# Kernel optimization log

Hardware: AMD Instinct MI355X
Metric: run time of the kernel (lower is better)

Reference implementation:

```python
import jax, jax.numpy as jnp
import numpy as np

B, N, CIN, CV, D, H, HD, W, SHIFT = 1024, 192, 63, 27, 256, 8, 32, 8, 4
DEPTH, MLP = 2, 256  # mlp_dim = int(embed_dim * mlp_ratio) = 256


def setup_inputs() -> dict:
    key = jax.random.key(0)
    ks = iter(jax.random.split(key, 64))
    def w(*shape):
        return jax.random.normal(next(ks), shape, jnp.float32) * 0.02
    z = lambda *s: jnp.zeros(s, jnp.float32)
    o = lambda *s: jnp.ones(s, jnp.float32)
    return {
        'input_pts': jax.random.normal(next(ks), (B, N, CIN), jnp.float32),
        'input_views': jax.random.normal(next(ks), (B, CV), jnp.float32),
        'w_in': w(CIN, D), 'b_in': z(D),
        'ln_in_s': o(D), 'ln_in_b': z(D),
        'ln1_s': o(DEPTH, D), 'ln1_b': z(DEPTH, D),
        'wq': w(DEPTH, D, H, HD), 'bq': z(DEPTH, H, HD),
        'wk': w(DEPTH, D, H, HD), 'bk': z(DEPTH, H, HD),
        'wv': w(DEPTH, D, H, HD), 'bv': z(DEPTH, H, HD),
        'wo': w(DEPTH, H, HD, D), 'bo': z(DEPTH, D),
        'ln2_s': o(DEPTH, D), 'ln2_b': z(DEPTH, D),
        'w_mlp1': w(DEPTH, D, MLP), 'b_mlp1': z(DEPTH, MLP),
        'w_mlp2': w(DEPTH, MLP, D), 'b_mlp2': z(DEPTH, D),
        'w_skip': w(DEPTH, CIN + D, D), 'b_skip': z(DEPTH, D),
        'ln_f_s': o(D), 'ln_f_b': z(D),
        'w_alpha': w(D, 1), 'b_alpha': z(1),
        'w_feat': w(D, D), 'b_feat': z(D),
        'w_rgb1': w(D + CV, D // 2), 'b_rgb1': z(D // 2),
        'w_rgb2': w(D // 2, 3), 'b_rgb2': z(3),
    }


def _ln(x, s, b, eps=1e-6):
    m = jnp.mean(x, -1, keepdims=True)
    v = jnp.mean(jnp.square(x - m), -1, keepdims=True)
    return (x - m) * jax.lax.rsqrt(v + eps) * s + b


def _pos_embed(n, d):
    pos = jnp.arange(n, dtype=jnp.float32)[:, None]
    i = jnp.arange(d)
    ang = pos / jnp.power(10000.0, (2 * (i // 2)).astype(jnp.float32) / d)
    return jnp.where(i % 2 == 0, jnp.sin(ang), jnp.cos(ang))[None]  # [1, n, d]


def _block(x, shifted, ln1_s, ln1_b, wq, bq, wk, bk, wv, bv, wo, bo,
           ln2_s, ln2_b, w1, b1, w2, b2):
    b, n, c = x.shape
    y = _ln(x, ln1_s, ln1_b)
    if shifted:
        y = jnp.roll(y, -SHIFT, axis=1)
    yw = y.reshape(b * (n // W), W, c)  # window partition
    q = jnp.einsum('bnc,chd->bnhd', yw, wq) + bq
    k = jnp.einsum('bnc,chd->bnhd', yw, wk) + bk
    v = jnp.einsum('bnc,chd->bnhd', yw, wv) + bv
    scale = np.float32(1.0 / np.sqrt(HD))
    a = jax.nn.softmax(jnp.einsum('bqhd,bkhd->bhqk', q * scale, k), axis=-1)
    o = jnp.einsum('bhqk,bkhd->bqhd', a, v)
    o = jnp.einsum('bqhd,hdc->bqc', o, wo) + bo
    o = o.reshape(b, n, c)  # window reverse
    if shifted:
        o = jnp.roll(o, SHIFT, axis=1)
    x = x + o
    y = _ln(x, ln2_s, ln2_b)
    y = jax.nn.gelu(jnp.einsum('bnc,cm->bnm', y, w1) + b1)
    y = jnp.einsum('bnm,mc->bnc', y, w2) + b2
    return x + y


def reference(input_pts, input_views, w_in, b_in, ln_in_s, ln_in_b,
              ln1_s, ln1_b, wq, bq, wk, bk, wv, bv, wo, bo, ln2_s, ln2_b,
              w_mlp1, b_mlp1, w_mlp2, b_mlp2, w_skip, b_skip,
              ln_f_s, ln_f_b, w_alpha, b_alpha, w_feat, b_feat,
              w_rgb1, b_rgb1, w_rgb2, b_rgb2):
    x = input_pts @ w_in + b_in
    x = _ln(x, ln_in_s, ln_in_b)
    x = x + _pos_embed(x.shape[1], x.shape[2])
    for i in range(DEPTH):  # shift on odd layers; skips = [0, 1]
        x = _block(x, i % 2 == 1, ln1_s[i], ln1_b[i], wq[i], bq[i], wk[i], bk[i],
                   wv[i], bv[i], wo[i], bo[i], ln2_s[i], ln2_b[i],
                   w_mlp1[i], b_mlp1[i], w_mlp2[i], b_mlp2[i])
        x = jax.nn.gelu(jnp.concatenate([input_pts, x], -1) @ w_skip[i] + b_skip[i])
    h = _ln(x, ln_f_s, ln_f_b)
    alpha = h @ w_alpha + b_alpha
    feature = h @ w_feat + b_feat
    views = jnp.repeat(input_views[:, None, :], h.shape[1], axis=1)
    hr = jnp.concatenate([feature, views], -1)
    rgb = jax.nn.gelu(hr @ w_rgb1 + b_rgb1) @ w_rgb2 + b_rgb2
    return rgb, alpha
```

## Files before the change

kernel.cpp:

```cpp
#include <hip/hip_runtime.h>
#include <hip/hip_bf16.h>
#include <math.h>

typedef __hip_bfloat16 bf16;
typedef __attribute__((ext_vector_type(8))) short short8;
typedef __attribute__((ext_vector_type(4))) float f32x4;

#define T_TOK 196608
#define NSEQ  192
#define DMODEL 256
#define CHUNKS 4
#define CHUNKM (T_TOK/CHUNKS)

__device__ __forceinline__ float cvt(float v){ return v; }
__device__ __forceinline__ float cvt(bf16 v){ return __bfloat162float(v); }
__device__ __forceinline__ short bfbits(float f){
  bf16 h = __float2bfloat16(f); return *reinterpret_cast<short*>(&h);
}
__device__ __forceinline__ float bfu(unsigned short v){ return __uint_as_float(((unsigned)v) << 16); }

__device__ __forceinline__ float gelu_f(float x){
  const float k0 = 0.7978845608028654f;
  float u = k0*(x + 0.044715f*x*x*x);
  return x / (1.f + __expf(-2.f*u));
}

__device__ __forceinline__ void barrier_lgkm(){
  asm volatile("s_waitcnt lgkmcnt(0)" ::: "memory");
  __builtin_amdgcn_s_barrier();
  asm volatile("" ::: "memory");
}

__global__ __launch_bounds__(256) void pe_kernel(float* __restrict__ PE){
  int n = blockIdx.x, d = threadIdx.x;
  float e = (float)(2*(d>>1)) / 256.f;
  float ang = (float)n * powf(10000.f, -e);
  PE[n*DMODEL + d] = (d & 1) ? cosf(ang) : sinf(ang);
}

__global__ __launch_bounds__(256) void w2b_kernel(
    const float* __restrict__ src, bf16* __restrict__ dst,
    int K, int N, int KL, int dstStride, int kOff, const float* __restrict__ scale)
{
  int idx = blockIdx.x*256 + threadIdx.x;
  if (idx >= N*KL) return;
  int n = idx / KL, k = idx - n*KL;
  float v = 0.f;
  if (k < K){
    v = src[(size_t)k*N + n];
    if (scale) v *= scale[k];
  }
  dst[(size_t)n*dstStride + kOff + k] = __float2bfloat16(v);
}

__global__ __launch_bounds__(256) void ucalc_kernel(
    const float* __restrict__ W, const float* __restrict__ lnS,
    const float* __restrict__ lnB, const float* __restrict__ bias,
    float* __restrict__ u, float* __restrict__ wB, int K, int N)
{
  __shared__ float pu[4], pb[4];
  const int n = blockIdx.x;
  const int k = threadIdx.x;
  float su = 0.f, sb = 0.f;
  if (k < K){
    float w = W[(size_t)k*N + n];
    su = cvt(__float2bfloat16(lnS[k]*w));
    sb = lnB[k]*w;
  }
  #pragma unroll
  for (int off = 32; off; off >>= 1){
    su += __shfl_xor(su, off, 64);
    sb += __shfl_xor(sb, off, 64);
  }
  int lane = k & 63, wv = k >> 6;
  if (lane == 0){ pu[wv] = su; pb[wv] = sb; }
  __syncthreads();
  if (k == 0){
    u[n]  = pu[0]+pu[1]+pu[2]+pu[3];
    wB[n] = pb[0]+pb[1]+pb[2]+pb[3] + bias[n];
  }
}

__global__ __launch_bounds__(256) void pts2b_kernel(
    const float* __restrict__ src, bf16* __restrict__ dst)
{
  int idx = blockIdx.x*256 + threadIdx.x;
  int t = idx >> 6, k = idx & 63;
  dst[idx] = __float2bfloat16(k < 63 ? src[(size_t)t*63 + k] : 0.f);
}

__global__ __launch_bounds__(256) void views2b_kernel(
    const float* __restrict__ src, bf16* __restrict__ dst)
{
  int idx = blockIdx.x*256 + threadIdx.x;
  int t = idx >> 5, k = idx & 31;
  dst[idx] = __float2bfloat16(k < 27 ? src[(size_t)t*27 + k] : 0.f);
}

__global__ __launch_bounds__(256) void ln_pe_kernel(
    bf16* __restrict__ X, const float* __restrict__ s, const float* __restrict__ b,
    const float* __restrict__ PE, float* __restrict__ s1o, float* __restrict__ s2o)
{
  const int lane = threadIdx.x & 63, w = threadIdx.x >> 6;
  const size_t t = (size_t)blockIdx.x * 4 + w;
  const int n = (int)(t % NSEQ);
  const int c = lane * 4;

  ushort4 u = *reinterpret_cast<const ushort4*>(X + t*DMODEL + c);
  float x0 = bfu(u.x), x1 = bfu(u.y), x2 = bfu(u.z), x3 = bfu(u.w);

  float sx = x0 + x1 + x2 + x3;
  float sq = x0*x0 + x1*x1 + x2*x2 + x3*x3;
  #pragma unroll
  for (int off = 32; off; off >>= 1){
    sx += __shfl_xor(sx, off, 64);
    sq += __shfl_xor(sq, off, 64);
  }
  float mean = sx * (1.f/256.f);
  float var  = sq * (1.f/256.f) - mean*mean;
  float rstd = rsqrtf(var + 1e-6f);

  float4 sv = *reinterpret_cast<const float4*>(s + c);
  float4 bv = *reinterpret_cast<const float4*>(b + c);
  float4 pv = *reinterpret_cast<const float4*>(PE + n*DMODEL + c);

  float y0 = (x0 - mean)*rstd*sv.x + bv.x + pv.x;
  float y1 = (x1 - mean)*rstd*sv.y + bv.y + pv.y;
  float y2 = (x2 - mean)*rstd*sv.z + bv.z + pv.z;
  float y3 = (x3 - mean)*rstd*sv.w + bv.w + pv.w;

  ushort4 o;
  o.x = (unsigned short)bfbits(y0);
  o.y = (unsigned short)bfbits(y1);
  o.z = (unsigned short)bfbits(y2);
  o.w = (unsigned short)bfbits(y3);
  *reinterpret_cast<ushort4*>(X + t*DMODEL + c) = o;

  float sy  = y0 + y1 + y2 + y3;
  float syq = y0*y0 + y1*y1 + y2*y2 + y3*y3;
  #pragma unroll
  for (int off = 32; off; off >>= 1){
    sy  += __shfl_xor(sy,  off, 64);
    syq += __shfl_xor(syq, off, 64);
  }
  if (lane == 0){ s1o[t] = sy; s2o[t] = syq; }
}

template<int MODE, bool LNF, bool ADD, bool GELU, bool STATS>
__global__ __launch_bounds__(256) void gemm_mfma(
    const bf16* __restrict__ A1, int lda1,
    const bf16* __restrict__ A2, int lda2, int SB, int aOff,
    const float* __restrict__ s1i, const float* __restrict__ s2i,
    const float* __restrict__ uvec,
    const bf16* __restrict__ WT, int Kpad, const float* __restrict__ bias,
    bf16* __restrict__ C, int ldc, size_t segStride, int cOff, int rollShift,
    float* __restrict__ s1o, float* __restrict__ s2o)
{
  __shared__ short buf[17408];
  short* As0 = buf;
  short* As1 = buf + 5120;
  short* Cs  = buf;
  __shared__ float sScale[128], sAlpha[128];

  const int tid = threadIdx.x;
  const int lane = tid & 63, wid = tid >> 6;
  const int wm = wid >> 1, wn = wid & 1;
  const int col16 = lane & 15, quad = lane >> 4;
  const int sm = tid >> 1, half = tid & 1;
  const int m0 = blockIdx.y * 128, n0 = blockIdx.x * 128;

  f32x4 acc[4][4];
  #pragma unroll
  for (int i = 0; i < 4; i++)
    #pragma unroll
    for (int j = 0; j < 4; j++) acc[i][j] = (f32x4){0.f,0.f,0.f,0.f};

  int row = m0 + sm;
  if (MODE == 0 && rollShift){
    int bb = row / NSEQ;
    int n  = row - bb*NSEQ;
    n += rollShift; if (n >= NSEQ) n -= NSEQ;
    row = bb*NSEQ + n;
  }
  const size_t arow = (size_t)aOff + row;
  const size_t arow2 = (MODE == 3) ? (arow / NSEQ) : arow;

  if (LNF && tid < 128){
    int r2 = m0 + tid;
    if (rollShift){
      int bb = r2 / NSEQ, n = r2 - bb*NSEQ;
      n += rollShift; if (n >= NSEQ) n -= NSEQ;
      r2 = bb*NSEQ + n;
    }
    size_t r = (size_t)aOff + r2;
    float m1 = s1i[r] * (1.f/256.f);
    float m2 = s2i[r] * (1.f/256.f);
    float rs = rsqrtf(m2 - m1*m1 + 1e-6f);
    sScale[tid] = rs;
    sAlpha[tid] = -m1*rs;
  }

  auto loadA = [&](int k0, uint4& u0, uint4& u1){
    const int gk = k0 + half*16;
    const bf16* src;
    if (MODE == 0) src = A1 + arow*(size_t)lda1 + gk;
    else src = (gk < SB) ? (A1 + arow*(size_t)lda1 + gk)
                         : (A2 + arow2*(size_t)lda2 + (gk - SB));
    u0 = *(const uint4*)(src);
    u1 = *(const uint4*)(src + 8);
  };
  auto writeA = [&](short* dst, const uint4& u0, const uint4& u1){
    *(uint4*)&dst[sm*40 + half*16]     = u0;
    *(uint4*)&dst[sm*40 + half*16 + 8] = u1;
  };

  uint4 p0, p1;
  loadA(0, p0, p1);
  writeA(As0, p0, p1);
  if (Kpad > 32) loadA(32, p0, p1);
  barrier_lgkm();

  int cur = 0;
  for (int k0 = 0; k0 < Kpad; k0 += 32){
    const short* Asc = cur ? As1 : As0;
    short8 afr[4];
    #pragma unroll
    for (int mi = 0; mi < 4; mi++)
      afr[mi] = *(const short8*)&Asc[(wm*64 + mi*16 + col16)*40 + quad*8];
    short8 bfr[4];
    #pragma unroll
    for (int ni = 0; ni < 4; ni++)
      bfr[ni] = *(const short8*)((const short*)WT
                 + (size_t)(n0 + wn*64 + ni*16 + col16)*Kpad + k0 + quad*8);
    #pragma unroll
    for (int mi = 0; mi < 4; mi++)
      #pragma unroll
      for (int ni = 0; ni < 4; ni++)
        acc[mi][ni] = __builtin_amdgcn_mfma_f32_16x16x32_bf16(
            afr[mi], bfr[ni], acc[mi][ni], 0, 0, 0);
    if (k0 + 32 < Kpad){
      short* Asn = cur ? As0 : As1;
      writeA(Asn, p0, p1);
      if (k0 + 64 < Kpad) loadA(k0+64, p0, p1);
    }
    barrier_lgkm();
    cur ^= 1;
  }

  #pragma unroll
  for (int ni = 0; ni < 4; ni++){
    int ncol = wn*64 + ni*16 + col16;
    float bv = bias[n0 + ncol];
    float uv = LNF ? uvec[n0 + ncol] : 0.f;
    #pragma unroll
    for (int mi = 0; mi < 4; mi++){
      f32x4 a = acc[mi][ni];
      #pragma unroll
      for (int r = 0; r < 4; r++){
        int lrow = wm*64 + mi*16 + quad*4 + r;
        float val;
        if (LNF) val = sScale[lrow]*a[r] + sAlpha[lrow]*uv + bv;
        else     val = a[r] + bv;
        if (GELU) val = gelu_f(val);
        Cs[lrow*136 + ncol] = bfbits(val);
      }
    }
  }
  __syncthreads();

  const int seg = n0 >> 8;
  const int nb  = n0 & 255;
  const int orow = tid >> 4;
  const int ocol = (tid & 15) * 8;
  #pragma unroll
  for (int p = 0; p < 8; p++){
    int lrow = p*16 + orow;
    size_t mrow = (size_t)cOff + m0 + lrow;
    short8 v = *(const short8*)&Cs[lrow*136 + ocol];
    bf16* dst = C + (size_t)seg*segStride + mrow*ldc + nb + ocol;
    float rowSum = 0.f, rowSq = 0.f;
    if (ADD){
      short8 c = *(const short8*)dst;
      short8 o;
      #pragma unroll
      for (int e = 0; e < 8; e++){
        bf16 va, ca;
        *reinterpret_cast<short*>(&va) = v[e];
        *reinterpret_cast<short*>(&ca) = c[e];
        float f = cvt(va) + cvt(ca);
        o[e] = bfbits(f);
        if (STATS){ rowSum += f; rowSq += f*f; }
      }
      *(short8*)dst = o;
    } else {
      if (STATS){
        #pragma unroll
        for (int e = 0; e < 8; e++){
          bf16 va; *reinterpret_cast<short*>(&va) = v[e];
          float f = cvt(va);
          rowSum += f; rowSq += f*f;
        }
      }
      *(short8*)dst = v;
    }
    if (STATS){
      #pragma unroll
      for (int mk = 1; mk <= 8; mk <<= 1){
        rowSum += __shfl_xor(rowSum, mk, 64);
        rowSq  += __shfl_xor(rowSq,  mk, 64);
      }
      if ((tid & 15) == 0){
        atomicAdd(&s1o[mrow], rowSum);
        atomicAdd(&s2o[mrow], rowSq);
      }
    }
  }
}

__global__ __launch_bounds__(256) void mlp_fused(
    const bf16* __restrict__ X,
    const float* __restrict__ s1i, const float* __restrict__ s2i,
    const float* __restrict__ uvec,
    const bf16* __restrict__ W1T,
    const float* __restrict__ wB1,
    const bf16* __restrict__ W2T,
    const float* __restrict__ b2,
    bf16* __restrict__ Y)
{
  __shared__ short sT[64*264];
  short* As0 = sT;
  short* As1 = sT + 2560;
  short* Cs  = sT;
  __shared__ float sScale[64], sAlpha[64];

  const int tid = threadIdx.x;
  const int lane = tid & 63, wid = tid >> 6;
  const int col16 = lane & 15, quad = lane >> 4;
  const int qr = tid >> 2, qc = tid & 3;
  const int m0 = blockIdx.x * 64;

  if (tid < 64){
    size_t r = (size_t)m0 + tid;
    float m1 = s1i[r] * (1.f/256.f);
    float m2 = s2i[r] * (1.f/256.f);
    float rs = rsqrtf(m2 - m1*m1 + 1e-6f);
    sScale[tid] = rs;
    sAlpha[tid] = -m1*rs;
  }

  const size_t arow = (size_t)m0 + qr;
  auto loadA = [&](int k0, uint4& u){
    u = *(const uint4*)(X + arow*DMODEL + k0 + qc*8);
  };
  auto writeA = [&](short* dst, const uint4& u){
    *(uint4*)&dst[qr*40 + qc*8] = u;
  };

  f32x4 acc[4][4];
  #pragma unroll
  for (int i = 0; i < 4; i++)
    #pragma unroll
    for (int j = 0; j < 4; j++) acc[i][j] = (f32x4){0.f,0.f,0.f,0.f};

  uint4 p;
  loadA(0, p); writeA(As0, p);
  loadA(32, p);
  barrier_lgkm();
  int cur = 0;
  for (int k0 = 0; k0 < 256; k0 += 32){
    const short* Asc = cur ? As1 : As0;
    short8 afr[4];
    #pragma unroll
    for (int mi = 0; mi < 4; mi++)
      afr[mi] = *(const short8*)&Asc[(mi*16 + col16)*40 + quad*8];
    short8 bfr[4];
    #pragma unroll
    for (int ni = 0; ni < 4; ni++)
      bfr[ni] = *(const short8*)((const short*)W1T
                 + (size_t)(wid*64 + ni*16 + col16)*256 + k0 + quad*8);
    #pragma unroll
    for (int mi = 0; mi < 4; mi++)
      #pragma unroll
      for (int ni = 0; ni < 4; ni++)
        acc[mi][ni] = __builtin_amdgcn_mfma_f32_16x16x32_bf16(
            afr[mi], bfr[ni], acc[mi][ni], 0, 0, 0);
    if (k0 + 32 < 256){
      short* Asn = cur ? As0 : As1;
      writeA(Asn, p);
      if (k0 + 64 < 256) loadA(k0 + 64, p);
    }
    barrier_lgkm();
    cur ^= 1;
  }

  #pragma unroll
  for (int ni = 0; ni < 4; ni++){
    int ncol = wid*64 + ni*16 + col16;
    float uv = uvec[ncol];
    float bv = wB1[ncol];
    #pragma unroll
    for (int mi = 0; mi < 4; mi++){
      f32x4 a = acc[mi][ni];
      #pragma unroll
      for (int r = 0; r < 4; r++){
        int lrow = mi*16 + quad*4 + r;
        float val = sScale[lrow]*a[r] + sAlpha[lrow]*uv + bv;
        sT[lrow*264 + ncol] = bfbits(gelu_f(val));
      }
    }
  }
  __syncthreads();

  f32x4 acc2[4][4];
  #pragma unroll
  for (int i = 0; i < 4; i++)
    #pragma unroll
    for (int j = 0; j < 4; j++) acc2[i][j] = (f32x4){0.f,0.f,0.f,0.f};
  for (int k0 = 0; k0 < 256; k0 += 32){
    short8 afr[4];
    #pragma unroll
    for (int mi = 0; mi < 4; mi++)
      afr[mi] = *(const short8*)&sT[(mi*16 + col16)*264 + k0 + quad*8];
    short8 bfr[4];
    #pragma unroll
    for (int ni = 0; ni < 4; ni++)
      bfr[ni] = *(const short8*)((const short*)W2T
                 + (size_t)(wid*64 + ni*16 + col16)*256 + k0 + quad*8);
    #pragma unroll
    for (int mi = 0; mi < 4; mi++)
      #pragma unroll
      for (int ni = 0; ni < 4; ni++)
        acc2[mi][ni] = __builtin_amdgcn_mfma_f32_16x16x32_bf16(
            afr[mi], bfr[ni], acc2[mi][ni], 0, 0, 0);
  }
  __syncthreads();

  #pragma unroll
  for (int ni = 0; ni < 4; ni++){
    int ncol = wid*64 + ni*16 + col16;
    float bv = b2[ncol];
    #pragma unroll
    for (int mi = 0; mi < 4; mi++){
      f32x4 a = acc2[mi][ni];
      #pragma unroll
      for (int r = 0; r < 4; r++){
        int lrow = mi*16 + quad*4 + r;
        Cs[lrow*264 + ncol] = bfbits(a[r] + bv);
      }
    }
  }
  __syncthreads();

  const int orow = tid >> 5;
  const int oc   = (tid & 31) * 8;
  #pragma unroll
  for (int ppp = 0; ppp < 8; ppp++){
    int lrow = ppp*8 + orow;
    size_t mrow = (size_t)m0 + lrow;
    short8 v = *(const short8*)&Cs[lrow*264 + oc];
    bf16* dst = Y + mrow*DMODEL + oc;
    short8 c = *(const short8*)dst;
    short8 o;
    #pragma unroll
    for (int e = 0; e < 8; e++){
      bf16 va, ca;
      *reinterpret_cast<short*>(&va) = v[e];
      *reinterpret_cast<short*>(&ca) = c[e];
      o[e] = bfbits(cvt(va) + cvt(ca));
    }
    *(short8*)dst = o;
  }
}

__global__ __launch_bounds__(256) void attn_lite(
    bf16* __restrict__ Qg, const bf16* __restrict__ Kg, const bf16* __restrict__ Vg)
{
  __shared__ short Qs[16*264], Ks[16*264], Vs[16*264];
  __shared__ float sc[2*8*8*8];
  const int tid = threadIdx.x;
  const size_t base = (size_t)blockIdx.x * 16 * 256;

  #pragma unroll
  for (int it = 0; it < 2; it++){
    int c = it*256 + tid;
    int row = c >> 5, cb = (c & 31) * 8;
    size_t g = base + (size_t)row*256 + cb;
    *(uint4*)&Qs[row*264 + cb] = *(const uint4*)(Qg + g);
    *(uint4*)&Ks[row*264 + cb] = *(const uint4*)(Kg + g);
    *(uint4*)&Vs[row*264 + cb] = *(const uint4*)(Vg + g);
  }
  __syncthreads();

  const float scale = 0.17677669529663687f;
  if (tid < 128){
    int win = tid >> 6, h = (tid >> 3) & 7, qi = tid & 7;
    int qrow = win*8 + qi;
    short8 qv[4];
    #pragma unroll
    for (int j = 0; j < 4; j++)
      qv[j] = *(const short8*)&Qs[qrow*264 + h*32 + j*8];
    float s[8];
    #pragma unroll
    for (int k = 0; k < 8; k++){
      int krow = win*8 + k;
      float a = 0.f;
      #pragma unroll
      for (int j = 0; j < 4; j++){
        short8 kv = *(const short8*)&Ks[krow*264 + h*32 + j*8];
        #pragma unroll
        for (int e = 0; e < 8; e++)
          a += bfu((unsigned short)qv[j][e]) * bfu((unsigned short)kv[e]);
      }
      s[k] = a * scale;
    }
    float mx = s[0];
    #pragma unroll
    for (int k = 1; k < 8; k++) mx = fmaxf(mx, s[k]);
    float sum = 0.f;
    #pragma unroll
    for (int k = 0; k < 8; k++){ s[k] = __expf(s[k] - mx); sum += s[k]; }
    float inv = 1.f / sum;
    #pragma unroll
    for (int k = 0; k < 8; k++)
      sc[((win*8 + qi)*8 + h)*8 + k] = s[k] * inv;
  }
  __syncthreads();

  {
    const int c = tid, h = c >> 5;
    #pragma unroll
    for (int j = 0; j < 16; j++){
      int win = j >> 3, qi = j & 7;
      const float* pr = &sc[((win*8 + qi)*8 + h)*8];
      float o = 0.f;
      #pragma unroll
      for (int k = 0; k < 8; k++)
        o += pr[k] * bfu((unsigned short)Vs[(win*8 + k)*264 + c]);
      Qs[j*264 + c] = bfbits(o);
    }
  }
  __syncthreads();

  #pragma unroll
  for (int it = 0; it < 2; it++){
    int c = it*256 + tid;
    int row = c >> 5, cb = (c & 31) * 8;
    *(uint4*)(Qg + base + (size_t)row*256 + cb) = *(uint4*)&Qs[row*264 + cb];
  }
}

__global__ __launch_bounds__(256) void alpha_kernel(
    const bf16* __restrict__ X, const float* __restrict__ s1,
    const float* __restrict__ s2, const float* __restrict__ s,
    const float* __restrict__ b, const float* __restrict__ wa,
    const float* __restrict__ ba, float* __restrict__ out)
{
  int lane = threadIdx.x & 63, w = threadIdx.x >> 6;
  size_t t = (size_t)blockIdx.x * 4 + w;
  float m = s1[t] * (1.f/256.f);
  float q = s2[t] * (1.f/256.f);
  float r = rsqrtf(q - m*m + 1e-6f);
  float acc = 0.f;
  #pragma unroll
  for (int j = 0; j < 4; j++){
    int c = lane + 64*j;
    float y = (cvt(X[t*DMODEL + c]) - m) * r * s[c] + b[c];
    acc += y * wa[c];
  }
  #pragma unroll
  for (int off = 32; off; off >>= 1) acc += __shfl_down(acc, off, 64);
  if (lane == 0) out[t] = acc + ba[0];
}

__global__ __launch_bounds__(256) void rgb2_kernel(
    const bf16* __restrict__ T1, const float* __restrict__ w2,
    const float* __restrict__ b2, float* __restrict__ out)
{
  int lane = threadIdx.x & 63, w = threadIdx.x >> 6;
  size_t t = (size_t)blockIdx.x * 4 + w;
  float h0 = cvt(T1[t*256 + lane]);
  float h1 = cvt(T1[t*256 + 64 + lane]);
  float a0 = h0*w2[lane*3+0] + h1*w2[(lane+64)*3+0];
  float a1 = h0*w2[lane*3+1] + h1*w2[(lane+64)*3+1];
  float a2 = h0*w2[lane*3+2] + h1*w2[(lane+64)*3+2];
  #pragma unroll
  for (int off = 32; off; off >>= 1){
    a0 += __shfl_down(a0, off, 64);
    a1 += __shfl_down(a1, off, 64);
    a2 += __shfl_down(a2, off, 64);
  }
  if (lane == 0){
    out[t*3+0] = a0 + b2[0];
    out[t*3+1] = a1 + b2[1];
    out[t*3+2] = a2 + b2[2];
  }
}

extern "C" void kernel_launch(void* const* d_in, const int* in_sizes, int n_in,
                              void* d_out, int out_size, void* d_ws, size_t ws_size,
                              hipStream_t stream)
{
  (void)in_sizes; (void)n_in; (void)out_size;
  const float* pts     = (const float*)d_in[0];
  const float* views   = (const float*)d_in[1];
  const float* w_in    = (const float*)d_in[2];
  const float* b_in    = (const float*)d_in[3];
  const float* ln_in_s = (const float*)d_in[4];
  const float* ln_in_b = (const float*)d_in[5];
  const float* ln1_s   = (const float*)d_in[6];
  const float* ln1_b   = (const float*)d_in[7];
  const float* wq      = (const float*)d_in[8];
  const float* bq      = (const float*)d_in[9];
  const float* wk      = (const float*)d_in[10];
  const float* bk      = (const float*)d_in[11];
  const float* wv      = (const float*)d_in[12];
  const float* bv      = (const float*)d_in[13];
  const float* wo      = (const float*)d_in[14];
  const float* bo      = (const float*)d_in[15];
  const float* ln2_s   = (const float*)d_in[16];
  const float* ln2_b   = (const float*)d_in[17];
  const float* w_mlp1  = (const float*)d_in[18];
  const float* b_mlp1  = (const float*)d_in[19];
  const float* w_mlp2  = (const float*)d_in[20];
  const float* b_mlp2  = (const float*)d_in[21];
  const float* w_skip  = (const float*)d_in[22];
  const float* b_skip  = (const float*)d_in[23];
  const float* ln_f_s  = (const float*)d_in[24];
  const float* ln_f_b  = (const float*)d_in[25];
  const float* w_alpha = (const float*)d_in[26];
  const float* b_alpha = (const float*)d_in[27];
  const float* w_feat  = (const float*)d_in[28];
  const float* b_feat  = (const float*)d_in[29];
  const float* w_rgb1  = (const float*)d_in[30];
  const float* b_rgb1  = (const float*)d_in[31];
  const float* w_rgb2  = (const float*)d_in[32];
  const float* b_rgb2  = (const float*)d_in[33];

  const size_t SZ = (size_t)T_TOK * DMODEL * 2;
  const size_t WT_ELEMS = 16384 + 2*(196608 + 3*65536 + 81920) + 65536 + 36864;
  const size_t UV_FLOATS = 2*768*2 + 2*256*2 + 2*256;
  const size_t NEED = 2*SZ + (size_t)4*T_TOK*4 + NSEQ*DMODEL*4 + UV_FLOATS*4
                    + WT_ELEMS*2 + (size_t)T_TOK*64*2 + 1024*32*2;
  if (ws_size < NEED) return;

  char* wsp = (char*)d_ws;
  bf16* xr = (bf16*)(wsp);
  bf16* x2 = (bf16*)(wsp + SZ);
  float* s1A = (float*)(wsp + 2*SZ);
  float* s2A = s1A + T_TOK;
  float* s1B = s2A + T_TOK;
  float* s2B = s1B + T_TOK;
  float* PE  = s2B + T_TOK;
  float* uvp = PE + NSEQ*DMODEL;
  float* uqkv[2], *wBqkv[2], *um1[2], *wBm1[2];
  {
    float* q = uvp;
    for (int i = 0; i < 2; i++){ uqkv[i] = q; q += 768; }
    for (int i = 0; i < 2; i++){ wBqkv[i] = q; q += 768; }
    for (int i = 0; i < 2; i++){ um1[i] = q; q += 256; }
    for (int i = 0; i < 2; i++){ wBm1[i] = q; q += 256; }
  }
  float* ufeat  = uvp + 2*768*2 + 2*256*2;
  float* wBfeat = ufeat + 256;
  bf16* wtp = (bf16*)(uvp + UV_FLOATS);

  bf16* wt_in = wtp;
  bf16* wt_qkv[2], *wt_o[2], *wt_m1[2], *wt_m2[2], *wt_sk[2];
  bf16* p = wt_in + 16384;
  for (int i = 0; i < 2; i++){
    wt_qkv[i] = p; p += 196608;
    wt_o[i]   = p; p += 65536;
    wt_m1[i]  = p; p += 65536;
    wt_m2[i]  = p; p += 65536;
    wt_sk[i]  = p; p += 81920;
  }
  bf16* wt_feat = p; p += 65536;
  bf16* wt_rgb1 = p; p += 36864;
  bf16* pts_b   = p; p += (size_t)T_TOK*64;
  bf16* views_b = p; p += 1024*32;

  float* out_rgb   = (float*)d_out;
  float* out_alpha = out_rgb + (size_t)T_TOK * 3;

  dim3 blk(256);
  dim3 g256(2, T_TOK/128);
  dim3 gQKV(6, CHUNKM/128);
  dim3 gC(2, CHUNKM/128);
  dim3 g128(1, T_TOK/128);
  dim3 gLN(T_TOK/4);
  dim3 gMLP(T_TOK/64);
  dim3 gStat(T_TOK/4);
  dim3 gAttn(CHUNKM/16);

  const float* NF = nullptr;
  const bf16*  NB = nullptr;
  float* NFW = nullptr;

  pe_kernel<<<dim3(NSEQ), blk, 0, stream>>>(PE);
  pts2b_kernel<<<dim3(T_TOK*64/256), blk, 0, stream>>>(pts, pts_b);
  views2b_kernel<<<dim3(1024*32/256), blk, 0, stream>>>(views, views_b);
  #define W2B(src, dst, K_, N_, KL_, ST_, KO_, SC_) \
    w2b_kernel<<<dim3(((N_)*(KL_)+255)/256), blk, 0, stream>>>(src, dst, K_, N_, KL_, ST_, KO_, SC_)
  W2B(w_in, wt_in, 63, 256, 64, 64, 0, NF);
  for (int i = 0; i < 2; i++){
    const float* s1 = ln1_s + i*256;
    const float* b1 = ln1_b + i*256;
    W2B(wq + (size_t)i*65536, wt_qkv[i],            256, 256, 256, 256, 0, s1);
    W2B(wk + (size_t)i*65536, wt_qkv[i] + 65536,    256, 256, 256, 256, 0, s1);
    W2B(wv + (size_t)i*65536, wt_qkv[i] + 131072,   256, 256, 256, 256, 0, s1);
    ucalc_kernel<<<dim3(256), blk, 0, stream>>>(wq + (size_t)i*65536, s1, b1,
        bq + i*256, uqkv[i],       wBqkv[i],       256, 256);
    ucalc_kernel<<<dim3(256), blk, 0, stream>>>(wk + (size_t)i*65536, s1, b1,
        bk + i*256, uqkv[i] + 256, wBqkv[i] + 256, 256, 256);
    ucalc_kernel<<<dim3(256), blk, 0, stream>>>(wv + (size_t)i*65536, s1, b1,
        bv + i*256, uqkv[i] + 512, wBqkv[i] + 512, 256, 256);
    W2B(wo + (size_t)i*65536, wt_o[i],  256, 256, 256, 256, 0, NF);
    W2B(w_mlp1 + (size_t)i*65536, wt_m1[i], 256, 256, 256, 256, 0, ln2_s + i*256);
    ucalc_kernel<<<dim3(256), blk, 0, stream>>>(w_mlp1 + (size_t)i*65536,
        ln2_s + i*256, ln2_b + i*256, b_mlp1 + i*256, um1[i], wBm1[i], 256, 256);
    W2B(w_mlp2 + (size_t)i*65536, wt_m2[i], 256, 256, 256, 256, 0, NF);
    W2B(w_skip + (size_t)i*81664,            wt_sk[i], 63, 256, 64, 320, 0, NF);
    W2B(w_skip + (size_t)i*81664 + 63*256,   wt_sk[i], 256, 256, 256, 320, 64, NF);
  }
  W2B(w_feat, wt_feat, 256, 256, 256, 256, 0, ln_f_s);
  ucalc_kernel<<<dim3(256), blk, 0, stream>>>(w_feat, ln_f_s, ln_f_b, b_feat,
      ufeat, wBfeat, 256, 256);
  W2B(w_rgb1,                wt_rgb1, 256, 128, 256, 288, 0, NF);
  W2B(w_rgb1 + 256*128,      wt_rgb1, 27, 128, 32, 288, 256, NF);
  #undef W2B

  gemm_mfma<0,false,false,false,false><<<g256, blk, 0, stream>>>(pts_b, 64,
      NB, 0, 0, 0, NF, NF, NF, wt_in, 64, b_in,
      xr, 256, 0, 0, 0, NFW, NFW);
  ln_pe_kernel<<<gLN, blk, 0, stream>>>(xr, ln_in_s, ln_in_b, PE, s1A, s2A);

  for (int i = 0; i < 2; i++){
    const int shift = (i == 1) ? 4 : 0;
    const int shiftBack = (i == 1) ? (NSEQ - 4) : 0;

    hipMemsetAsync(s1B, 0, (size_t)2*T_TOK*4, stream);

    bf16* qb = x2;
    bf16* kb = x2 + (size_t)CHUNKM * 256;
    bf16* vb = x2 + (size_t)2 * CHUNKM * 256;
    for (int cch = 0; cch < CHUNKS; cch++){
      int base = cch * CHUNKM;
      gemm_mfma<0,true,false,false,false><<<gQKV, blk, 0, stream>>>(xr, 256,
          NB, 0, 0, base, s1A, s2A, uqkv[i], wt_qkv[i], 256, wBqkv[i],
          x2, 256, (size_t)CHUNKM*256, 0, shift, NFW, NFW);
      attn_lite<<<gAttn, blk, 0, stream>>>(qb, kb, vb);
      gemm_mfma<0,false,true,false,true><<<gC, blk, 0, stream>>>(qb, 256,
          NB, 0, 0, 0, NF, NF, NF, wt_o[i], 256, bo + i*256,
          xr, 256, 0, base, shiftBack, s1B, s2B);
    }

    mlp_fused<<<gMLP, blk, 0, stream>>>(xr, s1B, s2B, um1[i],
        wt_m1[i], wBm1[i], wt_m2[i], b_mlp2 + i*256, xr);

    hipMemsetAsync(s1A, 0, (size_t)2*T_TOK*4, stream);
    gemm_mfma<2,false,false,true,true><<<g256, blk, 0, stream>>>(pts_b, 64,
        xr, 256, 64, 0, NF, NF, NF, wt_sk[i], 320, b_skip + i*256,
        x2, 256, 0, 0, 0, s1A, s2A);
    bf16* tmp = xr; xr = x2; x2 = tmp;
  }

  alpha_kernel<<<gStat, blk, 0, stream>>>(xr, s1A, s2A, ln_f_s, ln_f_b,
      w_alpha, b_alpha, out_alpha);
  gemm_mfma<0,true,false,false,false><<<g256, blk, 0, stream>>>(xr, 256,
      NB, 0, 0, 0, s1A, s2A, ufeat, wt_feat, 256, wBfeat,
      x2, 256, 0, 0, 0, NFW, NFW);
  gemm_mfma<3,false,false,true,false><<<g128, blk, 0, stream>>>(x2, 256,
      views_b, 32, 256, 0, NF, NF, NF, wt_rgb1, 288, b_rgb1,
      xr, 256, 0, 0, 0, NFW, NFW);
  rgb2_kernel<<<gStat, blk, 0, stream>>>(xr, w_rgb2, b_rgb2, out_rgb);
}
```

Measured before the change: 1.905 ms.

## Fuse skip-projection GEMM and LN stats into the MLP kernel

The MLP kernel now keeps the residual sum (x + MLP output) in shared memory and immediately runs the skip GEMM over [pts, x] with a GELU epilogue. It writes the result and per-row LayerNorm sums directly, without atomics or a memset. This removes a full write and re-read of the residual tensor, one kernel launch and a memset. In exchange the fused kernel does more work per block, and its skip GEMM reads B fragments straight from global memory without LDS staging, which may hurt occupancy or efficiency.

```diff
diff --git a/kernel.cpp b/kernel.cpp
--- a/kernel.cpp
+++ b/kernel.cpp
@@ -317,15 +317,19 @@
   }
 }
 
-__global__ __launch_bounds__(256) void mlp_fused(
+__global__ __launch_bounds__(256) void mlp_skip_fused(
     const bf16* __restrict__ X,
+    const bf16* __restrict__ PTS,
     const float* __restrict__ s1i, const float* __restrict__ s2i,
     const float* __restrict__ uvec,
     const bf16* __restrict__ W1T,
     const float* __restrict__ wB1,
     const bf16* __restrict__ W2T,
     const float* __restrict__ b2,
-    bf16* __restrict__ Y)
+    const bf16* __restrict__ WSK,
+    const float* __restrict__ bsk,
+    bf16* __restrict__ Z,
+    float* __restrict__ s1o, float* __restrict__ s2o)
 {
   __shared__ short sT[64*264];
   short* As0 = sT;
@@ -338,6 +342,8 @@
   const int col16 = lane & 15, quad = lane >> 4;
   const int qr = tid >> 2, qc = tid & 3;
   const int m0 = blockIdx.x * 64;
+  const int orow = tid >> 5;
+  const int oc   = (tid & 31) * 8;
 
   if (tid < 64){
     size_t r = (size_t)m0 + tid;
@@ -445,30 +451,97 @@
       #pragma unroll
       for (int r = 0; r < 4; r++){
         int lrow = mi*16 + quad*4 + r;
-        Cs[lrow*264 + ncol] = bfbits(a[r] + bv);
+        sT[lrow*264 + ncol] = bfbits(a[r] + bv);
       }
     }
   }
   __syncthreads();
 
-  const int orow = tid >> 5;
-  const int oc   = (tid & 31) * 8;
-  #pragma unroll
-  for (int ppp = 0; ppp < 8; ppp++){
-    int lrow = ppp*8 + orow;
+  #pragma unroll
+  for (int pp = 0; pp < 8; pp++){
+    int lrow = pp*8 + orow;
+    short8 xv = *(const short8*)(X + ((size_t)m0 + lrow)*DMODEL + oc);
+    short8 tv = *(const short8*)&sT[lrow*264 + oc];
+    short8 o;
+    #pragma unroll
+    for (int e = 0; e < 8; e++)
+      o[e] = bfbits(bfu((unsigned short)xv[e]) + bfu((unsigned short)tv[e]));
+    *(short8*)&sT[lrow*264 + oc] = o;
+  }
+  __syncthreads();
+
+  const bf16* pp4[4];
+  #pragma unroll
+  for (int mi = 0; mi < 4; mi++)
+    pp4[mi] = PTS + (size_t)(m0 + mi*16 + col16)*64 + quad*8;
+
+  f32x4 acc3[4][4];
+  #pragma unroll
+  for (int i = 0; i < 4; i++)
+    #pragma unroll
+    for (int j = 0; j < 4; j++) acc3[i][j] = (f32x4){0.f,0.f,0.f,0.f};
+  for (int k0 = 0; k0 < 320; k0 += 32){
+    short8 afr[4];
+    if (k0 < 64){
+      #pragma unroll
+      for (int mi = 0; mi < 4; mi++)
+        afr[mi] = *(const short8*)(pp4[mi] + k0);
+    } else {
+      #pragma unroll
+      for (int mi = 0; mi < 4; mi++)
+        afr[mi] = *(const short8*)&sT[(mi*16 + col16)*264 + (k0 - 64) + quad*8];
+    }
+    short8 bfr[4];
+    #pragma unroll
+    for (int ni = 0; ni < 4; ni++)
+      bfr[ni] = *(const short8*)((const short*)WSK
+                 + (size_t)(wid*64 + ni*16 + col16)*320 + k0 + quad*8);
+    #pragma unroll
+    for (int mi = 0; mi < 4; mi++)
+      #pragma unroll
+      for (int ni = 0; ni < 4; ni++)
+        acc3[mi][ni] = __builtin_amdgcn_mfma_f32_16x16x32_bf16(
+            afr[mi], bfr[ni], acc3[mi][ni], 0, 0, 0);
+  }
+  __syncthreads();
+
+  #pragma unroll
+  for (int ni = 0; ni < 4; ni++){
+    int ncol = wid*64 + ni*16 + col16;
+    float bv = bsk[ncol];
+    #pragma unroll
+    for (int mi = 0; mi < 4; mi++){
+      f32x4 a = acc3[mi][ni];
+      #pragma unroll
+      for (int r = 0; r < 4; r++){
+        int lrow = mi*16 + quad*4 + r;
+        Cs[lrow*264 + ncol] = bfbits(gelu_f(a[r] + bv));
+      }
+    }
+  }
+  __syncthreads();
+
+  #pragma unroll
+  for (int pp = 0; pp < 8; pp++){
+    int lrow = pp*8 + orow;
     size_t mrow = (size_t)m0 + lrow;
     short8 v = *(const short8*)&Cs[lrow*264 + oc];
-    bf16* dst = Y + mrow*DMODEL + oc;
-    short8 c = *(const short8*)dst;
-    short8 o;
+    float rowSum = 0.f, rowSq = 0.f;
     #pragma unroll
     for (int e = 0; e < 8; e++){
-      bf16 va, ca;
-      *reinterpret_cast<short*>(&va) = v[e];
-      *reinterpret_cast<short*>(&ca) = c[e];
-      o[e] = bfbits(cvt(va) + cvt(ca));
-    }
-    *(short8*)dst = o;
+      float f = bfu((unsigned short)v[e]);
+      rowSum += f; rowSq += f*f;
+    }
+    *(short8*)(Z + mrow*DMODEL + oc) = v;
+    #pragma unroll
+    for (int mk = 1; mk <= 16; mk <<= 1){
+      rowSum += __shfl_xor(rowSum, mk, 64);
+      rowSq  += __shfl_xor(rowSq,  mk, 64);
+    }
+    if ((tid & 31) == 0){
+      s1o[mrow] = rowSum;
+      s2o[mrow] = rowSq;
+    }
   }
 }
 
@@ -754,13 +827,9 @@
           xr, 256, 0, base, shiftBack, s1B, s2B);
     }
 
-    mlp_fused<<<gMLP, blk, 0, stream>>>(xr, s1B, s2B, um1[i],
-        wt_m1[i], wBm1[i], wt_m2[i], b_mlp2 + i*256, xr);
-
-    hipMemsetAsync(s1A, 0, (size_t)2*T_TOK*4, stream);
-    gemm_mfma<2,false,false,true,true><<<g256, blk, 0, stream>>>(pts_b, 64,
-        xr, 256, 64, 0, NF, NF, NF, wt_sk[i], 320, b_skip + i*256,
-        x2, 256, 0, 0, 0, s1A, s2A);
+    mlp_skip_fused<<<gMLP, blk, 0, stream>>>(xr, pts_b, s1B, s2B, um1[i],
+        wt_m1[i], wBm1[i], wt_m2[i], b_mlp2 + i*256,
+        wt_sk[i], b_skip + i*256, x2, s1A, s2A);
     bf16* tmp = xr; xr = x2; x2 = tmp;
   }
 
```

Result: no change. 1.869 ms (median of 2 runs) (-1.9%).
